# Kernel optimization log

Measured on AMD Instinct MI355X. Metric: run time of the kernel, lower is better.

Reference implementation:

```python
import jax, jax.numpy as jnp
import numpy as np

B, T, D = 4, 2048, 1024
H = 16
DH = D // H

def setup_inputs() -> dict:
    key = jax.random.key(0)
    k1, k2, k3 = jax.random.split(key, 3)
    x = jax.random.normal(k1, (B, T, D), dtype=jnp.float32)
    causal_mask = jnp.tril(jnp.ones((T, T), dtype=bool))[None, None]  # (1,1,T,T)
    Wqkv = jax.random.normal(k2, (D, 3 * D), dtype=jnp.float32) * (1.0 / np.sqrt(D))
    Wout = jax.random.normal(k3, (D, D), dtype=jnp.float32) * (1.0 / np.sqrt(D))
    return {"x": x, "causal_mask": causal_mask, "Wqkv": Wqkv, "Wout": Wout}

def reference(x, causal_mask, Wqkv, Wout):
    Bb, Tt, C = x.shape
    scale = jnp.sqrt(jnp.asarray(DH, dtype=x.dtype))
    qkv = x @ Wqkv                                   # (B,T,3D)
    qkv = qkv.reshape(Bb, Tt, 3, H, DH)
    qkv = jnp.transpose(qkv, (2, 0, 3, 1, 4))        # (3,B,H,T,DH)
    q, k, v = qkv[0], qkv[1], qkv[2]
    attn = jnp.einsum('bhqd,bhkd->bhqk', q, k) / scale
    attn = jnp.where(causal_mask, attn, jnp.asarray(-jnp.inf, dtype=attn.dtype))
    attn = jax.nn.softmax(attn, axis=-1)             # dropout p=0 -> identity
    out = jnp.einsum('bhqk,bhkd->bhqd', attn, v)     # (B,H,T,DH)
    out = jnp.transpose(out, (0, 2, 1, 3)).reshape(Bb, Tt, C)
    return out @ Wout
```

## Files before the change

### kernel.cpp

```cpp
#include <hip/hip_runtime.h>
#include <hip/hip_bf16.h>
#include <math.h>


#define Bb 4
#define Tt 2048
#define Dd 1024
#define Hh 16
#define DH 64
#define Mrows (Bb*Tt)
#define NEGBIG (-1.0e30f)
#define KB64 (Dd/64)
#define KB32 (Dd/32)
#define CHUNKS 1024
#define TILEU16 8192

typedef unsigned short u16;
typedef __attribute__((ext_vector_type(8))) short bf16x8;
typedef __attribute__((ext_vector_type(4))) float f32x4;
typedef __attribute__((ext_vector_type(4))) unsigned int u32x4;

__device__ __forceinline__ u16 f2bf(float f) {
    union { float f; unsigned int i; } v; v.f = f;
    unsigned int x = v.i;
    return (u16)((x + 0x7fffu + ((x >> 16) & 1u)) >> 16);
}

__device__ __forceinline__ unsigned int cvt_pk_bf16(float lo, float hi) {
    unsigned int r;
    asm("v_cvt_pk_bf16_f32 %0, %1, %2" : "=v"(r) : "v"(lo), "v"(hi));
    return r;
}

__device__ __forceinline__ void perm32swap(unsigned& x, unsigned& y) {
    asm("v_permlane32_swap_b32 %0, %1" : "+v"(x), "+v"(y));
}
__device__ __forceinline__ void perm16swap(unsigned& x, unsigned& y) {
    asm("v_permlane16_swap_b32 %0, %1" : "+v"(x), "+v"(y));
}

__device__ __forceinline__ float exp2_(float x) {
#if __has_builtin(__builtin_amdgcn_exp2f)
    return __builtin_amdgcn_exp2f(x);
#else
    return __expf(x * 0.69314718056f);
#endif
}

typedef __attribute__((address_space(1))) const void glob_cv;
typedef __attribute__((address_space(3))) void lds_v;
__device__ __forceinline__ void gl2lds16(const void* g, void* l) {
    __builtin_amdgcn_global_load_lds((glob_cv*)g, (lds_v*)l, 16, 0, 0);
}

__device__ __forceinline__ void conv_w_body(const float* __restrict__ W,
                                            u16* __restrict__ Wt, int N,
                                            int nb, int kb, int tid,
                                            u16 (*t)[68]) {
    const int k0 = kb * 64, n0 = nb * 128;
    const int k = tid >> 2, ng = tid & 3;
    const float* s = W + (size_t)(k0 + k) * N + n0 + ng * 32;
    #pragma unroll
    for (int i = 0; i < 8; ++i) {
        float4 f = *(const float4*)(s + i * 4);
        const int n = ng * 32 + i * 4;
        t[n + 0][k] = f2bf(f.x); t[n + 1][k] = f2bf(f.y);
        t[n + 2][k] = f2bf(f.z); t[n + 3][k] = f2bf(f.w);
    }
    __syncthreads();
    u16* base = Wt + (size_t)(nb * KB64 + kb) * TILEU16;
    #pragma unroll
    for (int it = 0; it < 4; ++it) {
        const int c = it * 256 + tid;
        const int row = c & 127, kq = c >> 7;
        union { u16 u[8]; uint4 v; } o;
        #pragma unroll
        for (int j = 0; j < 8; ++j) o.u[j] = t[row][kq * 8 + j];
        *(uint4*)(base + (size_t)c * 8) = o.v;
    }
}

__global__ __launch_bounds__(256) void convert_all(const float* __restrict__ x,
                                                   const float* __restrict__ Wqkv,
                                                   const float* __restrict__ Wout,
                                                   u16* __restrict__ xT,
                                                   u16* __restrict__ WqkvT,
                                                   u16* __restrict__ WoutT) {
    __shared__ u16 t[128][68];
    const int bid = blockIdx.x, tid = threadIdx.x;
    if (bid < 1024) {
        const int mb = bid >> 4, kb = bid & 15;
        const int row = tid & 127, half = tid >> 7;
        const float* s = x + (size_t)(mb * 128 + row) * Dd + kb * 64 + half * 32;
        u16* base = xT + (size_t)bid * TILEU16;
        #pragma unroll
        for (int cq = 0; cq < 4; ++cq) {
            const int kq = half * 4 + cq;
            float4 f0 = *(const float4*)(s + cq * 8);
            float4 f1 = *(const float4*)(s + cq * 8 + 4);
            uint4 o;
            o.x = cvt_pk_bf16(f0.x, f0.y); o.y = cvt_pk_bf16(f0.z, f0.w);
            o.z = cvt_pk_bf16(f1.x, f1.y); o.w = cvt_pk_bf16(f1.z, f1.w);
            *(uint4*)(base + (size_t)(kq * 128 + row) * 8) = o;
        }
    } else if (bid < 1408) {
        const int r = bid - 1024;
        conv_w_body(Wqkv, WqkvT, 3 * Dd, r % 24, r / 24, tid, t);
    } else {
        const int r = bid - 1408;
        conv_w_body(Wout, WoutT, Dd, r % 8, r / 8, tid, t);
    }
}

template <int MODE>
__global__ __launch_bounds__(512, 4) void gemm_mfma(const u16* __restrict__ At,
                                                    const u16* __restrict__ Bt,
                                                    u16* __restrict__ Qo,
                                                    u16* __restrict__ KT,
                                                    u16* __restrict__ VtT,
                                                    float* __restrict__ Out) {
    __shared__ u16 As[3][2][4 * 128 * 8];
    __shared__ u16 Bs[3][4 * 128 * 8];

    const int tid  = threadIdx.x;
    const int lane = tid & 63, w = tid >> 6;
    const int ml   = lane & 15, q = lane >> 4;
    const int wm   = w >> 1, wn = w & 1;
    const int mh   = wm >> 1;
    const int mrow = (wm & 1) * 64;

    const int nbx = gridDim.x;
    const int nwg = nbx * gridDim.y;
    int id = blockIdx.y * nbx + blockIdx.x;
    id = (id & 7) * (nwg >> 3) + (id >> 3);
    const int bxs = id % nbx, bys = id / nbx;

    const u16* A0 = At + (size_t)(2 * bys)     * KB64 * TILEU16;
    const u16* A1 = At + (size_t)(2 * bys + 1) * KB64 * TILEU16;
    const u16* B0 = Bt + (size_t)bxs           * KB64 * TILEU16;

    f32x4 acc[4][4];
    #pragma unroll
    for (int i = 0; i < 4; ++i)
        #pragma unroll
        for (int j = 0; j < 4; ++j) acc[i][j] = (f32x4){0.f, 0.f, 0.f, 0.f};

    #define STAGE_A32(k_, sl_, it_) do {                                      \
        const int c_ = (it_) * 512 + tid;                        \
        const int h_ = c_ >> 9, cc_ = c_ & 511;                               \
        gl2lds16((h_ ? A1 : A0) + (size_t)((k_) >> 1) * TILEU16 +             \
                 ((k_) & 1) * 4096 + (size_t)cc_ * 8,                         \
                 (char*)As[sl_][h_] + (size_t)cc_ * 16);                      \
    } while (0)
    #define STAGE_B32(k_, sl_) do {                                          \
        gl2lds16(B0 + (size_t)((k_) >> 1) * TILEU16 +                         \
                 ((k_) & 1) * 4096 + (size_t)tid * 8,                         \
                 (char*)Bs[sl_] + (size_t)tid * 16);                          \
    } while (0)

    STAGE_A32(0, 0, 0); STAGE_A32(0, 0, 1); STAGE_B32(0, 0);
    STAGE_A32(1, 1, 0); STAGE_A32(1, 1, 1); STAGE_B32(1, 1);

    for (int k = 0; k < KB32; ++k) {
        const int sl = k % 3;
        if (k == KB32 - 1) asm volatile("s_waitcnt vmcnt(0)" ::: "memory");
        else               asm volatile("s_waitcnt vmcnt(3)" ::: "memory");
        __builtin_amdgcn_s_barrier();

        const int k2 = k + 2, s2 = k2 % 3;
        if (k2 < KB32) { STAGE_A32(k2, s2, 0); STAGE_A32(k2, s2, 1); STAGE_B32(k2, s2); }

        bf16x8 bfr[4], af[4];
        #pragma unroll
        for (int j = 0; j < 4; ++j)
            bfr[j] = *(const bf16x8*)((const char*)Bs[sl] +
                    ((q * 128) + wn * 64 + j * 16 + ml) * 16);
        #pragma unroll
        for (int i = 0; i < 4; ++i)
            af[i] = *(const bf16x8*)((const char*)As[sl][mh] +
                    ((q * 128) + mrow + i * 16 + ml) * 16);

        __builtin_amdgcn_s_setprio(1);
        #pragma unroll
        for (int i = 0; i < 4; ++i)
            #pragma unroll
            for (int j = 0; j < 4; ++j)
                acc[i][j] = __builtin_amdgcn_mfma_f32_16x16x32_bf16(
                        bfr[j], af[i], acc[i][j], 0, 0, 0);
        __builtin_amdgcn_s_setprio(0);
    }
    #undef STAGE_A32
    #undef STAGE_B32

    if (MODE == 0) {
        const int s  = (bxs * 128) >> 10;
        const int h0 = ((bxs * 128) & 1023) >> 6;
        #pragma unroll
        for (int i = 0; i < 4; ++i) {
            const int m  = bys * 256 + wm * 64 + i * 16 + ml;
            const int bb = m >> 11, t = m & 2047;
            const int bhn = bb * Hh + h0 + wn;
            #pragma unroll
            for (int j = 0; j < 4; ++j) {
                const int dh = j * 16 + q * 4;
                if (s == 2) {
                    u16* vb = VtT + (size_t)(bhn * 16 + (t >> 7)) * TILEU16;
                    #pragma unroll
                    for (int r = 0; r < 4; ++r)
                        vb[(size_t)(((t >> 3) & 15) * 64 + dh + r) * 8 + (t & 7)]
                            = f2bf(acc[i][j][r]);
                } else if (s == 1) {
                    uint2 pk;
                    pk.x = cvt_pk_bf16(acc[i][j][0], acc[i][j][1]);
                    pk.y = cvt_pk_bf16(acc[i][j][2], acc[i][j][3]);
                    *(uint2*)(KT + (size_t)(bhn * 16 + (t >> 7)) * TILEU16 +
                              (size_t)((j * 2 + (q >> 1)) * 128 + (t & 127)) * 8 +
                              (q & 1) * 4) = pk;
                } else {
                    const float sc = 0.125f * 1.44269504089f;
                    uint2 pk;
                    pk.x = cvt_pk_bf16(acc[i][j][0] * sc, acc[i][j][1] * sc);
                    pk.y = cvt_pk_bf16(acc[i][j][2] * sc, acc[i][j][3] * sc);
                    *(uint2*)(Qo + ((size_t)bhn * Tt + t) * DH + dh) = pk;
                }
            }
        }
    } else {
        #pragma unroll
        for (int i = 0; i < 4; ++i) {
            const int m = bys * 256 + wm * 64 + i * 16 + ml;
            #pragma unroll
            for (int j = 0; j < 4; ++j) {
                const int n = bxs * 128 + wn * 64 + j * 16 + q * 4;
                float4 st = {acc[i][j][0], acc[i][j][1], acc[i][j][2], acc[i][j][3]};
                *(float4*)(Out + (size_t)m * Dd + n) = st;
            }
        }
    }
}

__device__ __forceinline__ void softmax_pack(f32x4 (&st)[8], float& l_i,
                                             unsigned (&d)[8], unsigned (&e)[8],
                                             int q, int qrow, bool diag) {
    if (diag) {
        #pragma unroll
        for (int kt = 0; kt < 8; ++kt)
            #pragma unroll
            for (int r = 0; r < 4; ++r)
                if (kt * 16 + q * 4 + r > qrow) st[kt][r] = NEGBIG;
    }
    float rs = 0.f;
    #pragma unroll
    for (int kt = 0; kt < 8; ++kt) {
        const float p0 = exp2_(st[kt][0]);
        const float p1 = exp2_(st[kt][1]);
        const float p2 = exp2_(st[kt][2]);
        const float p3 = exp2_(st[kt][3]);
        rs += (p0 + p1) + (p2 + p3);
        d[kt] = cvt_pk_bf16(p0, p1);
        e[kt] = cvt_pk_bf16(p2, p3);
    }
    rs += __shfl_xor(rs, 16, 64);
    rs += __shfl_xor(rs, 32, 64);
    l_i += rs;
}

__device__ __forceinline__ bf16x8 build_bp(const unsigned (&d)[8],
                                           const unsigned (&e)[8], int s) {
    unsigned w0 = d[2 * s], w2 = d[2 * s + 1];
    perm32swap(w0, w2); perm16swap(w0, w2);
    unsigned w1 = e[2 * s], w3 = e[2 * s + 1];
    perm32swap(w1, w3); perm16swap(w1, w3);
    union { u32x4 u; bf16x8 b; } cv;
    cv.u = (u32x4){w0, w1, w2, w3};
    return cv.b;
}

__global__ __launch_bounds__(256, 3) void attn_mfma(const u16* __restrict__ Q,
                                                    const u16* __restrict__ KT,
                                                    const u16* __restrict__ VtT,
                                                    u16* __restrict__ AOT) {
    __shared__ u16 Ks[8 * 128 * 8];
    __shared__ u16 Vs[2][16 * 64 * 8];

    const int tid  = threadIdx.x;
    const int lane = tid & 63, w = tid >> 6;
    const int nl   = lane & 15, q = lane >> 4;

    int id = blockIdx.y * 8 + blockIdx.x;
    id = (id & 7) * 64 + (id >> 3);
    const int bxp = id & 7, bh = id >> 3;
    const int b = bh >> 4, h = bh & 15;
    const size_t kbase = (size_t)bh * Tt * DH;

    for (int phase = 0; phase < 2; ++phase) {
        const int qt = phase ? (15 - bxp) : bxp;
        const int q0 = qt * 128;
        const int nj = qt + 1;

        bf16x8 qf[2][2];
        #pragma unroll
        for (int qb = 0; qb < 2; ++qb)
            #pragma unroll
            for (int s = 0; s < 2; ++s)
                qf[qb][s] = *(const bf16x8*)(Q + kbase +
                        (size_t)(q0 + w * 32 + qb * 16 + nl) * DH + (s * 4 + q) * 8);

        float l_i[2] = {0.f, 0.f};
        f32x4 accO[2][4];
        #pragma unroll
        for (int qb = 0; qb < 2; ++qb)
            #pragma unroll
            for (int dt = 0; dt < 4; ++dt) accO[qb][dt] = (f32x4){0.f, 0.f, 0.f, 0.f};

        __syncthreads();
        {
            const u16* Kb = KT  + (size_t)(bh * 16) * TILEU16;
            const u16* Vb = VtT + (size_t)(bh * 16) * TILEU16;
            #pragma unroll
            for (int it = 0; it < 4; ++it) {
                const int c = it * 256 + tid;
                gl2lds16(Kb + (size_t)c * 8, (char*)Ks + c * 16);
                gl2lds16(Vb + (size_t)c * 8, (char*)Vs[0] + c * 16);
            }
        }

        for (int jt = 0; jt < nj; ++jt) {
            const int buf = jt & 1;
            __syncthreads();

            f32x4 st0[8], st1[8];
            #pragma unroll
            for (int kt = 0; kt < 8; ++kt) {
                st0[kt] = (f32x4){0.f, 0.f, 0.f, 0.f};
                st1[kt] = (f32x4){0.f, 0.f, 0.f, 0.f};
            }
            __builtin_amdgcn_s_setprio(1);
            #pragma unroll
            for (int s = 0; s < 2; ++s) {
                #pragma unroll
                for (int kt = 0; kt < 8; ++kt) {
                    bf16x8 ak = *(const bf16x8*)((const char*)Ks +
                            ((s * 4 + q) * 128 + kt * 16 + nl) * 16);
                    st0[kt] = __builtin_amdgcn_mfma_f32_16x16x32_bf16(
                            ak, qf[0][s], st0[kt], 0, 0, 0);
                    st1[kt] = __builtin_amdgcn_mfma_f32_16x16x32_bf16(
                            ak, qf[1][s], st1[kt], 0, 0, 0);
                }
            }
            __builtin_amdgcn_s_setprio(0);

            __syncthreads();

            if (jt + 1 < nj) {
                const u16* Kb = KT  + (size_t)(bh * 16 + jt + 1) * TILEU16;
                const u16* Vb = VtT + (size_t)(bh * 16 + jt + 1) * TILEU16;
                #pragma unroll
                for (int it = 0; it < 4; ++it) {
                    const int c = it * 256 + tid;
                    gl2lds16(Kb + (size_t)c * 8, (char*)Ks + c * 16);
                    gl2lds16(Vb + (size_t)c * 8, (char*)Vs[buf ^ 1] + c * 16);
                }
            }

            const bool diag = (jt == nj - 1);
            unsigned d0[8], e0[8], d1[8], e1[8];
            softmax_pack(st0, l_i[0], d0, e0, q, w * 32 + nl, diag);
            softmax_pack(st1, l_i[1], d1, e1, q, w * 32 + 16 + nl, diag);

            __builtin_amdgcn_s_setprio(1);
            #pragma unroll
            for (int s = 0; s < 4; ++s) {
                bf16x8 bp0 = build_bp(d0, e0, s);
                bf16x8 bp1 = build_bp(d1, e1, s);
                #pragma unroll
                for (int dt = 0; dt < 4; ++dt) {
                    bf16x8 av = *(const bf16x8*)((const char*)Vs[buf] +
                            ((s * 4 + q) * 64 + dt * 16 + nl) * 16);
                    accO[0][dt] = __builtin_amdgcn_mfma_f32_16x16x32_bf16(
                            av, bp0, accO[0][dt], 0, 0, 0);
                    accO[1][dt] = __builtin_amdgcn_mfma_f32_16x16x32_bf16(
                            av, bp1, accO[1][dt], 0, 0, 0);
                }
            }
            __builtin_amdgcn_s_setprio(0);
        }

        #pragma unroll
        for (int qb = 0; qb < 2; ++qb) {
            const float inv = 1.0f / l_i[qb];
            const int t = q0 + w * 32 + qb * 16 + nl;
            const int m = b * Tt + t;
            u16* ab = AOT + (size_t)((m >> 7) * KB64 + h) * TILEU16;
            #pragma unroll
            for (int dt = 0; dt < 4; ++dt) {
                uint2 pk;
                pk.x = cvt_pk_bf16(accO[qb][dt][0] * inv, accO[qb][dt][1] * inv);
                pk.y = cvt_pk_bf16(accO[qb][dt][2] * inv, accO[qb][dt][3] * inv);
                *(uint2*)(ab + (size_t)((dt * 2 + (q >> 1)) * 128 + (m & 127)) * 8 +
                          (q & 1) * 4) = pk;
            }
        }
    }
}

extern "C" void kernel_launch(void* const* d_in, const int* in_sizes, int n_in,
                              void* d_out, int out_size, void* d_ws, size_t ws_size,
                              hipStream_t stream) {
    const float* x_raw    = (const float*)d_in[0];
    const float* Wqkv_raw = (const float*)d_in[2];
    const float* Wout_raw = (const float*)d_in[3];
    float* out = (float*)d_out;

    const size_t SZ = (size_t)Bb * Hh * Tt * DH;
    u16* ws = (u16*)d_ws;
    u16* Qw     = ws;
    u16* KT     = ws + SZ;
    u16* VtT    = ws + 2 * SZ;
    u16* AOT    = ws + 3 * SZ;
    u16* WqkvT  = ws + 4 * SZ;
    u16* WoutT  = WqkvT + (size_t)3 * Dd * Dd;
    u16* xT     = (u16*)d_out;

    convert_all<<<dim3(1536), 256, 0, stream>>>(x_raw, Wqkv_raw, Wout_raw,
                                                xT, WqkvT, WoutT);
    gemm_mfma<0><<<dim3(3 * Dd / 128, Mrows / 256), 512, 0, stream>>>(xT, WqkvT, Qw, KT, VtT, nullptr);
    attn_mfma  <<<dim3(Tt / 256, Bb * Hh), 256, 0, stream>>>(Qw, KT, VtT, AOT);
    gemm_mfma<1><<<dim3(Dd / 128, Mrows / 256), 512, 0, stream>>>(AOT, WoutT, nullptr, nullptr, nullptr, out);
}
```

Baseline: 260.1 us.

## Enlarge GEMM block tile to 256x256 with split-phase double-buffered LDS staging

The projection GEMM now computes a 256x256 output tile per workgroup instead of 256x128. Its 8 waves are arranged 2x4, each holding a 128x64 accumulator. The triple-buffered 32-wide K pipeline becomes a double-buffered 64-wide K step split into four sub-phases, each with its own barrier and partial prefetch of the next A/B slices. The larger tile raises arithmetic intensity and cuts global/LDS traffic per FLOP. In exchange it halves the number of workgroups (only 128 for the output projection on a 256-CU device), lowers the occupancy target to 2, and roughly doubles accumulator registers.

```diff
diff --git a/kernel.cpp b/kernel.cpp
--- a/kernel.cpp
+++ b/kernel.cpp
@@ -11,7 +11,6 @@
 #define Mrows (Bb*Tt)
 #define NEGBIG (-1.0e30f)
 #define KB64 (Dd/64)
-#define KB32 (Dd/32)
 #define CHUNKS 1024
 #define TILEU16 8192
 
@@ -113,21 +112,20 @@
 }
 
 template <int MODE>
-__global__ __launch_bounds__(512, 4) void gemm_mfma(const u16* __restrict__ At,
+__global__ __launch_bounds__(512, 2) void gemm_mfma(const u16* __restrict__ At,
                                                     const u16* __restrict__ Bt,
                                                     u16* __restrict__ Qo,
                                                     u16* __restrict__ KT,
                                                     u16* __restrict__ VtT,
                                                     float* __restrict__ Out) {
-    __shared__ u16 As[3][2][4 * 128 * 8];
-    __shared__ u16 Bs[3][4 * 128 * 8];
+    __shared__ u16 As[2][2][8192];
+    __shared__ u16 Bs[2][2][8192];
 
     const int tid  = threadIdx.x;
     const int lane = tid & 63, w = tid >> 6;
     const int ml   = lane & 15, q = lane >> 4;
-    const int wm   = w >> 1, wn = w & 1;
-    const int mh   = wm >> 1;
-    const int mrow = (wm & 1) * 64;
+    const int wm   = w >> 2, wn = w & 3;
+    const int bh_  = wn >> 1, bcol = (wn & 1) * 64;
 
     const int nbx = gridDim.x;
     const int nwg = nbx * gridDim.y;
@@ -135,51 +133,43 @@
     id = (id & 7) * (nwg >> 3) + (id >> 3);
     const int bxs = id % nbx, bys = id / nbx;
 
-    const u16* A0 = At + (size_t)(2 * bys)     * KB64 * TILEU16;
-    const u16* A1 = At + (size_t)(2 * bys + 1) * KB64 * TILEU16;
-    const u16* B0 = Bt + (size_t)bxs           * KB64 * TILEU16;
-
-    f32x4 acc[4][4];
+    const u16* Ab0 = At + (size_t)(2 * bys)     * KB64 * TILEU16;
+    const u16* Ab1 = At + (size_t)(2 * bys + 1) * KB64 * TILEU16;
+    const u16* Bb0 = Bt + (size_t)(2 * bxs)     * KB64 * TILEU16;
+    const u16* Bb1 = Bt + (size_t)(2 * bxs + 1) * KB64 * TILEU16;
+
+    f32x4 acc[8][4];
     #pragma unroll
-    for (int i = 0; i < 4; ++i)
+    for (int i = 0; i < 8; ++i)
         #pragma unroll
         for (int j = 0; j < 4; ++j) acc[i][j] = (f32x4){0.f, 0.f, 0.f, 0.f};
 
-    #define STAGE_A32(k_, sl_, it_) do {                                      \
-        const int c_ = (it_) * 512 + tid;                        \
-        const int h_ = c_ >> 9, cc_ = c_ & 511;                               \
-        gl2lds16((h_ ? A1 : A0) + (size_t)((k_) >> 1) * TILEU16 +             \
-                 ((k_) & 1) * 4096 + (size_t)cc_ * 8,                         \
-                 (char*)As[sl_][h_] + (size_t)cc_ * 16);                      \
-    } while (0)
-    #define STAGE_B32(k_, sl_) do {                                          \
-        gl2lds16(B0 + (size_t)((k_) >> 1) * TILEU16 +                         \
-                 ((k_) & 1) * 4096 + (size_t)tid * 8,                         \
-                 (char*)Bs[sl_] + (size_t)tid * 16);                          \
-    } while (0)
-
-    STAGE_A32(0, 0, 0); STAGE_A32(0, 0, 1); STAGE_B32(0, 0);
-    STAGE_A32(1, 1, 0); STAGE_A32(1, 1, 1); STAGE_B32(1, 1);
-
-    for (int k = 0; k < KB32; ++k) {
-        const int sl = k % 3;
-        if (k == KB32 - 1) asm volatile("s_waitcnt vmcnt(0)" ::: "memory");
-        else               asm volatile("s_waitcnt vmcnt(3)" ::: "memory");
+    #define STG(gb_, kb_, ks_, lb_)                                           \
+        gl2lds16((gb_) + (size_t)(kb_) * TILEU16 + (ks_) * 4096 +             \
+                 (size_t)tid * 8,                                             \
+                 (char*)(lb_) + (ks_) * 8192 + (size_t)tid * 16)
+
+    STG(Bb0, 0, 0, Bs[0][0]); STG(Bb1, 0, 0, Bs[0][1]);
+    STG(Ab0, 0, 0, As[0][0]); STG(Ab1, 0, 0, As[0][1]);
+    STG(Bb0, 0, 1, Bs[0][0]); STG(Bb1, 0, 1, Bs[0][1]);
+    STG(Ab0, 0, 1, As[0][0]); STG(Ab1, 0, 1, As[0][1]);
+
+    for (int kb = 0; kb < KB64; ++kb) {
+        const int db = kb & 1, dn = db ^ 1, kb1 = kb + 1;
+        const bool more = kb1 < KB64;
+        bf16x8 bfr[4], af[4];
+
+        asm volatile("s_waitcnt vmcnt(4)" ::: "memory");
         __builtin_amdgcn_s_barrier();
-
-        const int k2 = k + 2, s2 = k2 % 3;
-        if (k2 < KB32) { STAGE_A32(k2, s2, 0); STAGE_A32(k2, s2, 1); STAGE_B32(k2, s2); }
-
-        bf16x8 bfr[4], af[4];
+        if (more) { STG(Bb0, kb1, 0, Bs[dn][0]); STG(Bb1, kb1, 0, Bs[dn][1]); }
         #pragma unroll
         for (int j = 0; j < 4; ++j)
-            bfr[j] = *(const bf16x8*)((const char*)Bs[sl] +
-                    ((q * 128) + wn * 64 + j * 16 + ml) * 16);
-        #pragma unroll
-        for (int i = 0; i < 4; ++i)
-            af[i] = *(const bf16x8*)((const char*)As[sl][mh] +
-                    ((q * 128) + mrow + i * 16 + ml) * 16);
-
+            bfr[j] = *(const bf16x8*)((const char*)Bs[db][bh_] +
+                    ((q * 128) + bcol + j * 16 + ml) * 16);
+        #pragma unroll
+        for (int i = 0; i < 4; ++i)
+            af[i] = *(const bf16x8*)((const char*)As[db][wm] +
+                    ((q * 128) + i * 16 + ml) * 16);
         __builtin_amdgcn_s_setprio(1);
         #pragma unroll
         for (int i = 0; i < 4; ++i)
@@ -188,16 +178,70 @@
                 acc[i][j] = __builtin_amdgcn_mfma_f32_16x16x32_bf16(
                         bfr[j], af[i], acc[i][j], 0, 0, 0);
         __builtin_amdgcn_s_setprio(0);
-    }
-    #undef STAGE_A32
-    #undef STAGE_B32
+
+        if (more) asm volatile("s_waitcnt vmcnt(6)" ::: "memory");
+        else      asm volatile("s_waitcnt vmcnt(4)" ::: "memory");
+        __builtin_amdgcn_s_barrier();
+        if (more) { STG(Ab0, kb1, 0, As[dn][0]); STG(Ab1, kb1, 0, As[dn][1]); }
+        #pragma unroll
+        for (int i = 0; i < 4; ++i)
+            af[i] = *(const bf16x8*)((const char*)As[db][wm] +
+                    ((q * 128) + 64 + i * 16 + ml) * 16);
+        __builtin_amdgcn_s_setprio(1);
+        #pragma unroll
+        for (int i = 0; i < 4; ++i)
+            #pragma unroll
+            for (int j = 0; j < 4; ++j)
+                acc[i + 4][j] = __builtin_amdgcn_mfma_f32_16x16x32_bf16(
+                        bfr[j], af[i], acc[i + 4][j], 0, 0, 0);
+        __builtin_amdgcn_s_setprio(0);
+
+        if (more) asm volatile("s_waitcnt vmcnt(4)" ::: "memory");
+        else      asm volatile("s_waitcnt vmcnt(0)" ::: "memory");
+        __builtin_amdgcn_s_barrier();
+        if (more) { STG(Bb0, kb1, 1, Bs[dn][0]); STG(Bb1, kb1, 1, Bs[dn][1]); }
+        #pragma unroll
+        for (int j = 0; j < 4; ++j)
+            bfr[j] = *(const bf16x8*)((const char*)Bs[db][bh_] +
+                    (((4 + q) * 128) + bcol + j * 16 + ml) * 16);
+        #pragma unroll
+        for (int i = 0; i < 4; ++i)
+            af[i] = *(const bf16x8*)((const char*)As[db][wm] +
+                    (((4 + q) * 128) + i * 16 + ml) * 16);
+        __builtin_amdgcn_s_setprio(1);
+        #pragma unroll
+        for (int i = 0; i < 4; ++i)
+            #pragma unroll
+            for (int j = 0; j < 4; ++j)
+                acc[i][j] = __builtin_amdgcn_mfma_f32_16x16x32_bf16(
+                        bfr[j], af[i], acc[i][j], 0, 0, 0);
+        __builtin_amdgcn_s_setprio(0);
+
+        if (more) asm volatile("s_waitcnt vmcnt(6)" ::: "memory");
+        else      asm volatile("s_waitcnt vmcnt(0)" ::: "memory");
+        __builtin_amdgcn_s_barrier();
+        if (more) { STG(Ab0, kb1, 1, As[dn][0]); STG(Ab1, kb1, 1, As[dn][1]); }
+        #pragma unroll
+        for (int i = 0; i < 4; ++i)
+            af[i] = *(const bf16x8*)((const char*)As[db][wm] +
+                    (((4 + q) * 128) + 64 + i * 16 + ml) * 16);
+        __builtin_amdgcn_s_setprio(1);
+        #pragma unroll
+        for (int i = 0; i < 4; ++i)
+            #pragma unroll
+            for (int j = 0; j < 4; ++j)
+                acc[i + 4][j] = __builtin_amdgcn_mfma_f32_16x16x32_bf16(
+                        bfr[j], af[i], acc[i + 4][j], 0, 0, 0);
+        __builtin_amdgcn_s_setprio(0);
+    }
+    #undef STG
 
     if (MODE == 0) {
-        const int s  = (bxs * 128) >> 10;
-        const int h0 = ((bxs * 128) & 1023) >> 6;
-        #pragma unroll
-        for (int i = 0; i < 4; ++i) {
-            const int m  = bys * 256 + wm * 64 + i * 16 + ml;
+        const int s  = (bxs * 256) >> 10;
+        const int h0 = ((bxs * 256) & 1023) >> 6;
+        #pragma unroll
+        for (int i = 0; i < 8; ++i) {
+            const int m  = bys * 256 + wm * 128 + i * 16 + ml;
             const int bb = m >> 11, t = m & 2047;
             const int bhn = bb * Hh + h0 + wn;
             #pragma unroll
@@ -227,11 +271,11 @@
         }
     } else {
         #pragma unroll
-        for (int i = 0; i < 4; ++i) {
-            const int m = bys * 256 + wm * 64 + i * 16 + ml;
+        for (int i = 0; i < 8; ++i) {
+            const int m = bys * 256 + wm * 128 + i * 16 + ml;
             #pragma unroll
             for (int j = 0; j < 4; ++j) {
-                const int n = bxs * 128 + wn * 64 + j * 16 + q * 4;
+                const int n = bxs * 256 + wn * 64 + j * 16 + q * 4;
                 float4 st = {acc[i][j][0], acc[i][j][1], acc[i][j][2], acc[i][j][3]};
                 *(float4*)(Out + (size_t)m * Dd + n) = st;
             }
@@ -424,7 +468,7 @@
 
     convert_all<<<dim3(1536), 256, 0, stream>>>(x_raw, Wqkv_raw, Wout_raw,
                                                 xT, WqkvT, WoutT);
-    gemm_mfma<0><<<dim3(3 * Dd / 128, Mrows / 256), 512, 0, stream>>>(xT, WqkvT, Qw, KT, VtT, nullptr);
+    gemm_mfma<0><<<dim3(3 * Dd / 256, Mrows / 256), 512, 0, stream>>>(xT, WqkvT, Qw, KT, VtT, nullptr);
     attn_mfma  <<<dim3(Tt / 256, Bb * Hh), 256, 0, stream>>>(Qw, KT, VtT, AOT);
-    gemm_mfma<1><<<dim3(Dd / 128, Mrows / 256), 512, 0, stream>>>(AOT, WoutT, nullptr, nullptr, nullptr, out);
-}
+    gemm_mfma<1><<<dim3(Dd / 256, Mrows / 256), 512, 0, stream>>>(AOT, WoutT, nullptr, nullptr, nullptr, out);
+}
```

Result: slower. 298.3 us (+14.7%).
